# Optimization experiments

Hardware: AMD Instinct MI355X
Metric: run time of the kernel (lower is better)

The kernel has to match this reference:

```python
import jax, jax.numpy as jnp
import numpy as np

B, K, C = 1024, 8, 10   # predicted points, concepts, classes per concept
N = 8192                # background (training) set size
EPS = 1e-13


def setup_inputs() -> dict:
    key = jax.random.key(0)
    k1, k2, k3 = jax.random.split(key, 3)
    c_p = jax.random.normal(k1, (B, K, C), dtype=jnp.float32)
    bandwidth = jnp.ones((K * C,), dtype=jnp.float32)  # learned param, init 1.0
    c_in = jax.random.randint(k2, (N, K), 0, C, dtype=jnp.int64)
    delta_in = jax.random.randint(k3, (N,), 0, 2, dtype=jnp.int32)
    return {"c_p": c_p, "bandwidth": bandwidth, "c_in": c_in, "delta_in": delta_in}


def _beran(c_p, bandwidth, c_in, delta_in):
    # ---- GaussKernel l2 metric ----
    proba = jax.nn.softmax(c_p, axis=-1)                      # [B,K,C]
    bw = jnp.clip(bandwidth, 0.001, 10.0).reshape(K, C)       # [K,C]
    onehot = jax.nn.one_hot(c_in, C, dtype=proba.dtype)       # [N,K,C]
    # sum((p - l)^2 / bw) = sum(p^2/bw) - 2 sum(p*l/bw) + sum(l^2/bw)
    A = jnp.sum(proba * proba / bw, axis=(1, 2))              # [B]
    D = jnp.einsum('nkc,kc->n', onehot, 1.0 / bw)             # [N]
    cross = jnp.einsum('bkc,nkc->bn', proba / bw, onehot)     # [B,N]
    metric = A[:, None] - 2.0 * cross + D[None, :]            # [B,N]
    weights = jnp.exp(-metric)
    s = jnp.sum(weights, axis=1, keepdims=True)               # normalize over background axis
    bad = s < EPS
    W = jnp.where(bad, 0.0, weights / jnp.where(bad, 1.0, s)) # [B,N]

    # ---- Beran cumulative hazard scan ----
    w_cumsum = jnp.cumsum(W, axis=1)
    shifted = w_cumsum - W
    ones = jnp.ones_like(shifted)
    bad2 = jnp.isclose(shifted, ones) | jnp.isclose(w_cumsum, ones)
    shifted = jnp.where(bad2, 0.0, shifted)
    w_cumsum = jnp.where(bad2, 0.0, w_cumsum)
    xi = jnp.log(1.0 - shifted) - jnp.log(1.0 - w_cumsum)
    filtered_xi = delta_in.astype(xi.dtype)[None, :] * xi
    hazards = jnp.cumsum(filtered_xi, axis=1)
    surv_func = jnp.exp(-hazards)                             # [B,N]
    first_step = 1.0 - surv_func[:, :1]
    surv_steps = jnp.concatenate([first_step, surv_func[:, :-1] - surv_func[:, 1:]], axis=1)
    ss = jnp.sum(surv_steps, axis=1, keepdims=True)
    bad3 = ss < EPS
    surv_steps = jnp.where(bad3, 0.0, surv_steps / jnp.where(bad3, 1.0, ss))
    return surv_func, surv_steps


def reference(c_p, bandwidth, c_in, delta_in):
    return _beran(c_p, bandwidth, c_in, delta_in)
```

## Files before the change

### kernel.cpp

```cpp
#include <hip/hip_runtime.h>

#define NN 8192
#define BB 1024
#define KK 8
#define CC 10
#define NT 256
#define CHUNK (NN/NT)
#define NW (NT/64)

__device__ __forceinline__ int swz(int n) {
    return (n & ~31) | ((n + (n >> 5)) & 31);
}

__global__ void pack_kernel(const int* __restrict__ c_in, const int* __restrict__ delta_in,
                            uint2* __restrict__ packed, unsigned* __restrict__ dmask_g) {
    int n = blockIdx.x * blockDim.x + threadIdx.x;
    if (n >= NN) return;
    const int4* p = reinterpret_cast<const int4*>(c_in + (size_t)n * KK);
    int4 lo4 = p[0], hi4 = p[1];
    unsigned lo = (unsigned)(0*CC + lo4.x) | ((unsigned)(1*CC + lo4.y) << 8)
                | ((unsigned)(2*CC + lo4.z) << 16) | ((unsigned)(3*CC + lo4.w) << 24);
    unsigned hi = (unsigned)(4*CC + hi4.x) | ((unsigned)(5*CC + hi4.y) << 8)
                | ((unsigned)(6*CC + hi4.z) << 16) | ((unsigned)(7*CC + hi4.w) << 24);
    packed[n] = make_uint2(lo, hi);
    unsigned long long bal = __ballot(delta_in[n] & 1);
    if ((threadIdx.x & 63) == 0) {
        dmask_g[n >> 5]       = (unsigned)(bal & 0xffffffffull);
        dmask_g[(n >> 5) + 1] = (unsigned)(bal >> 32);
    }
}

__device__ __forceinline__ float block_excl_scan(float v, int lane, int wv, float* ws) {
    float x = v;
    #pragma unroll
    for (int d = 1; d < 64; d <<= 1) {
        float y = __shfl_up(x, d);
        if (lane >= d) x += y;
    }
    if (lane == 63) ws[wv] = x;
    __syncthreads();
    float woff = 0.0f;
    #pragma unroll
    for (int w = 0; w < NW - 1; w++)
        if (w < wv) woff += ws[w];
    return woff + (x - v);
}

__global__ __launch_bounds__(NT) void beran_kernel(
    const float* __restrict__ c_p, const float* __restrict__ bandwidth,
    const int* __restrict__ c_in, const int* __restrict__ delta_in,
    const uint2* __restrict__ packed, const unsigned* __restrict__ dmask_g,
    float* __restrict__ out)
{
    __shared__ float a[NN];
    __shared__ float ttab[KK * CC];
    __shared__ float Apart[KK];
    __shared__ float wsumS[NW];
    __shared__ float wsumB[NW];
    __shared__ float wsumC[NW];
    __shared__ unsigned dmls[NT];

    const int b    = blockIdx.x;
    const int t    = threadIdx.x;
    const int lane = t & 63;
    const int wv   = t >> 6;
    const int base = t * CHUNK;

    if (t < KK) {
        const int k = t;
        float v[CC];
        float mx = -1e30f;
        #pragma unroll
        for (int c = 0; c < CC; c++) { v[c] = c_p[((size_t)b*KK + k)*CC + c]; mx = fmaxf(mx, v[c]); }
        float se = 0.0f;
        #pragma unroll
        for (int c = 0; c < CC; c++) { v[c] = __expf(v[c] - mx); se += v[c]; }
        float inv = 1.0f / se;
        float Ak = 0.0f;
        #pragma unroll
        for (int c = 0; c < CC; c++) {
            float p  = v[c] * inv;
            float bw = bandwidth[k*CC + c];
            bw = fminf(fmaxf(bw, 0.001f), 10.0f);
            float ib = 1.0f / bw;
            ttab[k*CC + c] = ib - 2.0f * p * ib;
            Ak += p * p * ib;
        }
        Apart[k] = Ak;
    }
    __syncthreads();
    float A = 0.0f;
    #pragma unroll
    for (int k = 0; k < KK; k++) A += Apart[k];

    float lsum = 0.0f;
    unsigned dm;
    if (packed) {
        dm = dmask_g[t];
        for (int j = 0; j < CHUNK; j++) {
            int n = j * NT + t;
            uint2 pk = packed[n];
            float m = A;
            #pragma unroll
            for (int k = 0; k < 4; k++) m += ttab[(pk.x >> (8*k)) & 0xff];
            #pragma unroll
            for (int k = 0; k < 4; k++) m += ttab[(pk.y >> (8*k)) & 0xff];
            float w = __expf(-m);
            a[swz(n)] = w;
            lsum += w;
        }
    } else {
        for (int j = 0; j < CHUNK; j++) {
            int n = j * NT + t;
            unsigned long long bal = __ballot(delta_in[n] & 1);
            if (lane == 0) {
                dmls[(n >> 5)]     = (unsigned)(bal & 0xffffffffull);
                dmls[(n >> 5) + 1] = (unsigned)(bal >> 32);
            }
            const int4* p4 = reinterpret_cast<const int4*>(c_in + (size_t)n * KK);
            int4 lo4 = p4[0], hi4 = p4[1];
            float m = A;
            m += ttab[0*CC + lo4.x] + ttab[1*CC + lo4.y] + ttab[2*CC + lo4.z] + ttab[3*CC + lo4.w];
            m += ttab[4*CC + hi4.x] + ttab[5*CC + hi4.y] + ttab[6*CC + hi4.z] + ttab[7*CC + hi4.w];
            float w = __expf(-m);
            a[swz(n)] = w;
            lsum += w;
        }
    }

    float ws = lsum;
    #pragma unroll
    for (int d = 32; d; d >>= 1) ws += __shfl_xor(ws, d);
    if (lane == 0) wsumS[wv] = ws;
    __syncthreads();
    float s = wsumS[0] + wsumS[1] + wsumS[2] + wsumS[3];
    const float invs = (s < 1e-13f) ? 0.0f : 1.0f / s;
    if (!packed) dm = dmls[t];

    float creg[CHUNK];
    float run = 0.0f;
    #pragma unroll
    for (int i = 0; i < CHUNK; i++) { run += a[swz(base + i)]; creg[i] = run; }
    const float off_raw = block_excl_scan(run, lane, wv, wsumB);

    const float ISO = 1.00001e-5f;
    float csprev = off_raw * invs;
    float run2 = 0.0f;
    #pragma unroll
    for (int i = 0; i < CHUNK; i++) {
        float cs = (creg[i] + off_raw) * invs;
        bool bad = (fabsf(csprev - 1.0f) <= ISO) || (fabsf(cs - 1.0f) <= ISO);
        float xi = bad ? 0.0f : (__logf(1.0f - csprev) - __logf(1.0f - cs));
        float f  = ((dm >> i) & 1u) ? xi : 0.0f;
        run2 += f;
        creg[i] = run2;
        csprev = cs;
    }
    const float off2 = block_excl_scan(run2, lane, wv, wsumC);

    #pragma unroll
    for (int i = 0; i < CHUNK; i++) a[swz(base + i)] = __expf(-(creg[i] + off2));
    __syncthreads();

    const float surv_last = a[swz(NN - 1)];
    const float ss = 1.0f - surv_last;
    const float invss = (ss < 1e-13f) ? 0.0f : 1.0f / ss;
    float* outS = out + (size_t)b * NN;
    float* outT = out + (size_t)BB * NN + (size_t)b * NN;
    #pragma unroll
    for (int j = 0; j < NN / (NT * 4); j++) {
        int n0 = j * NT * 4 + t * 4;
        float s0 = a[swz(n0)];
        float s1 = a[swz(n0 + 1)];
        float s2 = a[swz(n0 + 2)];
        float s3 = a[swz(n0 + 3)];
        float sp = (n0 == 0) ? 1.0f : a[swz(n0 - 1)];
        float4 sv = make_float4(s0, s1, s2, s3);
        *reinterpret_cast<float4*>(outS + n0) = sv;
        float4 st = make_float4((sp - s0) * invss, (s0 - s1) * invss,
                                (s1 - s2) * invss, (s2 - s3) * invss);
        *reinterpret_cast<float4*>(outT + n0) = st;
    }
}

extern "C" void kernel_launch(void* const* d_in, const int* in_sizes, int n_in,
                              void* d_out, int out_size, void* d_ws, size_t ws_size,
                              hipStream_t stream) {
    const float* c_p       = (const float*)d_in[0];
    const float* bandwidth = (const float*)d_in[1];
    const int*   c_in      = (const int*)d_in[2];
    const int*   delta_in  = (const int*)d_in[3];
    float* out = (float*)d_out;

    uint2*    packed  = nullptr;
    unsigned* dmask_g = nullptr;
    const size_t need = (size_t)NN * sizeof(uint2) + (size_t)(NN / 32) * sizeof(unsigned);
    if (ws_size >= need) {
        packed  = (uint2*)d_ws;
        dmask_g = (unsigned*)((char*)d_ws + (size_t)NN * sizeof(uint2));
        pack_kernel<<<NN / NT, NT, 0, stream>>>(c_in, delta_in, packed, dmask_g);
    }
    beran_kernel<<<BB, NT, 0, stream>>>(c_p, bandwidth, c_in, delta_in, packed, dmask_g, out);
}
```

Measured before the change: 33.73 us.

## Use pairwise concept lookup tables, 512-thread blocks, and reuse log terms

Precomputes a 4x100 table of summed per-concept-pair terms so each background point needs four lookups from a single packed 32-bit word instead of eight from a uint2. The block size doubles to 512 threads, so each thread handles 16 elements and reads its delta mask as a 16-bit half-word. The hazard scan now reuses the previous element's log value, halving log evaluations per element. This adds an extra table-build step and barrier, and the larger blocks raise register pressure under launch bounds of 8.

```diff
diff --git a/kernel.cpp b/kernel.cpp
--- a/kernel.cpp
+++ b/kernel.cpp
@@ -4,7 +4,7 @@
 #define BB 1024
 #define KK 8
 #define CC 10
-#define NT 256
+#define NT 512
 #define CHUNK (NN/NT)
 #define NW (NT/64)
 
@@ -13,16 +13,16 @@
 }
 
 __global__ void pack_kernel(const int* __restrict__ c_in, const int* __restrict__ delta_in,
-                            uint2* __restrict__ packed, unsigned* __restrict__ dmask_g) {
+                            unsigned* __restrict__ pairs, unsigned* __restrict__ dmask_g) {
     int n = blockIdx.x * blockDim.x + threadIdx.x;
     if (n >= NN) return;
     const int4* p = reinterpret_cast<const int4*>(c_in + (size_t)n * KK);
-    int4 lo4 = p[0], hi4 = p[1];
-    unsigned lo = (unsigned)(0*CC + lo4.x) | ((unsigned)(1*CC + lo4.y) << 8)
-                | ((unsigned)(2*CC + lo4.z) << 16) | ((unsigned)(3*CC + lo4.w) << 24);
-    unsigned hi = (unsigned)(4*CC + hi4.x) | ((unsigned)(5*CC + hi4.y) << 8)
-                | ((unsigned)(6*CC + hi4.z) << 16) | ((unsigned)(7*CC + hi4.w) << 24);
-    packed[n] = make_uint2(lo, hi);
+    int4 lo = p[0], hi = p[1];
+    unsigned p0 = (unsigned)(lo.x * 10 + lo.y);
+    unsigned p1 = (unsigned)(lo.z * 10 + lo.w);
+    unsigned p2 = (unsigned)(hi.x * 10 + hi.y);
+    unsigned p3 = (unsigned)(hi.z * 10 + hi.w);
+    pairs[n] = p0 | (p1 << 7) | (p2 << 14) | (p3 << 21);
     unsigned long long bal = __ballot(delta_in[n] & 1);
     if ((threadIdx.x & 63) == 0) {
         dmask_g[n >> 5]       = (unsigned)(bal & 0xffffffffull);
@@ -46,19 +46,20 @@
     return woff + (x - v);
 }
 
-__global__ __launch_bounds__(NT) void beran_kernel(
+__global__ __launch_bounds__(NT, 8) void beran_kernel(
     const float* __restrict__ c_p, const float* __restrict__ bandwidth,
     const int* __restrict__ c_in, const int* __restrict__ delta_in,
-    const uint2* __restrict__ packed, const unsigned* __restrict__ dmask_g,
+    const unsigned* __restrict__ pairs, const unsigned* __restrict__ dmask_g,
     float* __restrict__ out)
 {
     __shared__ float a[NN];
     __shared__ float ttab[KK * CC];
+    __shared__ float ttab2[4 * 100];
     __shared__ float Apart[KK];
     __shared__ float wsumS[NW];
     __shared__ float wsumB[NW];
     __shared__ float wsumC[NW];
-    __shared__ unsigned dmls[NT];
+    __shared__ unsigned dmls[NN / 32];
 
     const int b    = blockIdx.x;
     const int t    = threadIdx.x;
@@ -89,22 +90,26 @@
         Apart[k] = Ak;
     }
     __syncthreads();
+    if (t < 400) {
+        int k = t / 100, p = t % 100;
+        ttab2[t] = ttab[(k*2)*CC + p/10] + ttab[(k*2+1)*CC + p%10];
+    }
     float A = 0.0f;
     #pragma unroll
     for (int k = 0; k < KK; k++) A += Apart[k];
+    __syncthreads();
 
     float lsum = 0.0f;
     unsigned dm;
-    if (packed) {
-        dm = dmask_g[t];
+    if (pairs) {
         for (int j = 0; j < CHUNK; j++) {
             int n = j * NT + t;
-            uint2 pk = packed[n];
+            unsigned pk = pairs[n];
             float m = A;
-            #pragma unroll
-            for (int k = 0; k < 4; k++) m += ttab[(pk.x >> (8*k)) & 0xff];
-            #pragma unroll
-            for (int k = 0; k < 4; k++) m += ttab[(pk.y >> (8*k)) & 0xff];
+            m += ttab2[pk & 127];
+            m += ttab2[100 + ((pk >> 7) & 127)];
+            m += ttab2[200 + ((pk >> 14) & 127)];
+            m += ttab2[300 + (pk >> 21)];
             float w = __expf(-m);
             a[swz(n)] = w;
             lsum += w;
@@ -128,14 +133,19 @@
         }
     }
 
-    float ws = lsum;
-    #pragma unroll
-    for (int d = 32; d; d >>= 1) ws += __shfl_xor(ws, d);
-    if (lane == 0) wsumS[wv] = ws;
-    __syncthreads();
-    float s = wsumS[0] + wsumS[1] + wsumS[2] + wsumS[3];
+    float wsr = lsum;
+    #pragma unroll
+    for (int d = 32; d; d >>= 1) wsr += __shfl_xor(wsr, d);
+    if (lane == 0) wsumS[wv] = wsr;
+    __syncthreads();
+    float s = 0.0f;
+    #pragma unroll
+    for (int w = 0; w < NW; w++) s += wsumS[w];
     const float invs = (s < 1e-13f) ? 0.0f : 1.0f / s;
-    if (!packed) dm = dmls[t];
+    {
+        unsigned dm32 = pairs ? dmask_g[t >> 1] : dmls[t >> 1];
+        dm = (dm32 >> ((t & 1) * 16)) & 0xffffu;
+    }
 
     float creg[CHUNK];
     float run = 0.0f;
@@ -145,16 +155,19 @@
 
     const float ISO = 1.00001e-5f;
     float csprev = off_raw * invs;
+    float Lprev  = __logf(1.0f - csprev);
     float run2 = 0.0f;
     #pragma unroll
     for (int i = 0; i < CHUNK; i++) {
         float cs = (creg[i] + off_raw) * invs;
+        float L  = __logf(1.0f - cs);
         bool bad = (fabsf(csprev - 1.0f) <= ISO) || (fabsf(cs - 1.0f) <= ISO);
-        float xi = bad ? 0.0f : (__logf(1.0f - csprev) - __logf(1.0f - cs));
+        float xi = bad ? 0.0f : (Lprev - L);
         float f  = ((dm >> i) & 1u) ? xi : 0.0f;
         run2 += f;
         creg[i] = run2;
         csprev = cs;
+        Lprev  = L;
     }
     const float off2 = block_excl_scan(run2, lane, wv, wsumC);
 
@@ -192,13 +205,13 @@
     const int*   delta_in  = (const int*)d_in[3];
     float* out = (float*)d_out;
 
-    uint2*    packed  = nullptr;
+    unsigned* pairs   = nullptr;
     unsigned* dmask_g = nullptr;
-    const size_t need = (size_t)NN * sizeof(uint2) + (size_t)(NN / 32) * sizeof(unsigned);
+    const size_t need = (size_t)NN * sizeof(unsigned) + (size_t)(NN / 32) * sizeof(unsigned);
     if (ws_size >= need) {
-        packed  = (uint2*)d_ws;
-        dmask_g = (unsigned*)((char*)d_ws + (size_t)NN * sizeof(uint2));
-        pack_kernel<<<NN / NT, NT, 0, stream>>>(c_in, delta_in, packed, dmask_g);
-    }
-    beran_kernel<<<BB, NT, 0, stream>>>(c_p, bandwidth, c_in, delta_in, packed, dmask_g, out);
-}
+        pairs   = (unsigned*)d_ws;
+        dmask_g = (unsigned*)((char*)d_ws + (size_t)NN * sizeof(unsigned));
+        pack_kernel<<<NN / 256, 256, 0, stream>>>(c_in, delta_in, pairs, dmask_g);
+    }
+    beran_kernel<<<BB, NT, 0, stream>>>(c_p, bandwidth, c_in, delta_in, pairs, dmask_g, out);
+}
```

Result: faster. 30.23 us (-10.4%).
